# Optimization experiments

Hardware: AMD Instinct MI355X
Metric: run time of the kernel (lower is better)

## Reference

```python
import jax, jax.numpy as jnp
import numpy as np

N_NODES = 100000
N_EDGES = 1600000
D_IN = 128
D_HID = 128
D_OUT = 10
N_GRAPHS = 512


def setup_inputs() -> dict:
    key = jax.random.key(0)
    ks = jax.random.split(key, 12)
    x = jax.random.normal(ks[0], (N_NODES, D_IN), dtype=jnp.float32)
    edge_index = jax.random.randint(ks[1], (2, N_EDGES), 0, N_NODES, dtype=jnp.int64)
    batch = jnp.sort(jax.random.randint(ks[2], (N_NODES,), 0, N_GRAPHS, dtype=jnp.int64))
    s = 1.0 / np.sqrt(D_HID)
    W0 = jax.random.normal(ks[3], (D_HID, D_IN), dtype=jnp.float32) * s
    b0 = jax.random.normal(ks[4], (D_HID,), dtype=jnp.float32) * s
    W1 = jax.random.normal(ks[5], (D_HID, D_HID), dtype=jnp.float32) * s
    b1 = jax.random.normal(ks[6], (D_HID,), dtype=jnp.float32) * s
    W2 = jax.random.normal(ks[7], (D_HID, D_HID), dtype=jnp.float32) * s
    b2 = jax.random.normal(ks[8], (D_HID,), dtype=jnp.float32) * s
    Wg = jax.random.normal(ks[9], (D_OUT, D_HID), dtype=jnp.float32) * s
    bg = jax.random.normal(ks[10], (D_OUT,), dtype=jnp.float32) * s
    return {"x": x, "edge_index": edge_index, "batch": batch,
            "W0": W0, "b0": b0, "W1": W1, "b1": b1, "W2": W2, "b2": b2,
            "Wg": Wg, "bg": bg}


def _gin_conv(x, src, dst, W, b):
    # GINConv with eps=0: Linear(x + sum_{j in N(i)} x_j)
    agg = jax.ops.segment_sum(x[src], dst, num_segments=N_NODES)  # [N, d]
    return (x + agg) @ W.T + b


def reference(x, edge_index, batch, W0, b0, W1, b1, W2, b2, Wg, bg):
    src, dst = edge_index[0], edge_index[1]
    h = jax.nn.relu(_gin_conv(x, src, dst, W0, b0))
    h = jax.nn.relu(_gin_conv(h, src, dst, W1, b1))
    h = _gin_conv(h, src, dst, W2, b2)
    # global_mean_pool over graph ids
    sums = jax.ops.segment_sum(h, batch, num_segments=N_GRAPHS)            # [G, d]
    counts = jax.ops.segment_sum(jnp.ones((N_NODES,), h.dtype), batch, num_segments=N_GRAPHS)
    pooled = sums / jnp.maximum(counts, 1.0)[:, None]                       # [G, d]
    return pooled @ Wg.T + bg                                               # [G, out]
```

## Files before the change

### kernel.cpp

```cpp
#include <hip/hip_runtime.h>

#define N_NODES 100000
#define N_EDGES 1600000
#define N_GRAPHS 512
#define NBUCK 391
#define EPB 8192
#define NB_SCAT ((N_EDGES + EPB - 1) / EPB)
#define CAPB 4864
#define CAP 5120
#define CONV_BLKS 6250
#define AGG_BLKS 2048

typedef _Float16 half8 __attribute__((ext_vector_type(8)));
typedef float floatx4 __attribute__((ext_vector_type(4)));

union U16 { uint4 u; half8 h; };

__global__ __launch_bounds__(256) void convert_pack(const float4* __restrict__ X4,
                                                    uint4* __restrict__ Xh,
                                                    const float* __restrict__ W0,
                                                    const float* __restrict__ W1,
                                                    const float* __restrict__ W2,
                                                    uint4* __restrict__ Bp) {
    int bid = blockIdx.x, tid = threadIdx.x;
    if (bid < CONV_BLKS) {
        int t = bid * 256 + tid;
        float4 a = X4[t * 2], b = X4[t * 2 + 1];
        U16 o;
        o.h[0] = (_Float16)a.x; o.h[1] = (_Float16)a.y;
        o.h[2] = (_Float16)a.z; o.h[3] = (_Float16)a.w;
        o.h[4] = (_Float16)b.x; o.h[5] = (_Float16)b.y;
        o.h[6] = (_Float16)b.z; o.h[7] = (_Float16)b.w;
        Xh[t] = o.u;
    } else {
        int slice = (bid - CONV_BLKS) * 4 + (tid >> 6);
        if (slice >= 96) return;
        int l = tid & 63;
        int layer = slice >> 5;
        int r = slice & 31;
        int c = r >> 3, f = r & 7;
        const float* W = (layer == 0) ? W0 : (layer == 1) ? W1 : W2;
        int col = f * 16 + (l & 15);
        int k0 = c * 32 + (l >> 4) * 8;
        U16 o;
        #pragma unroll
        for (int j = 0; j < 8; ++j) o.h[j] = (_Float16)W[col * 128 + k0 + j];
        Bp[layer * 2048 + (c * 8 + f) * 64 + l] = o.u;
    }
}

__global__ __launch_bounds__(256) void bucket_scatter(const int* __restrict__ src,
                                                      const int* __restrict__ dst,
                                                      int* __restrict__ gcur,
                                                      unsigned* __restrict__ pairs) {
    __shared__ int cnt[NBUCK];
    __shared__ int base[NBUCK];
    int tid = threadIdx.x;
    for (int i = tid; i < NBUCK; i += 256) cnt[i] = 0;
    __syncthreads();
    int e0 = blockIdx.x * EPB, e1 = min(e0 + EPB, N_EDGES);
    for (int e = e0 + tid; e < e1; e += 256) atomicAdd(&cnt[dst[e] >> 8], 1);
    __syncthreads();
    for (int i = tid; i < NBUCK; i += 256) {
        int v = cnt[i];
        base[i] = i * CAPB + (v ? atomicAdd(&gcur[i], v) : 0);
        cnt[i] = 0;
    }
    __syncthreads();
    for (int e = e0 + tid; e < e1; e += 256) {
        int d = dst[e], b = d >> 8;
        int r = atomicAdd(&cnt[b], 1);
        pairs[base[b] + r] = (unsigned)src[e] | ((unsigned)(d & 255) << 17);
    }
}

__global__ __launch_bounds__(256) void bucket_fine(const unsigned* __restrict__ pairs,
                                                   const int* __restrict__ gcur,
                                                   int* __restrict__ off,
                                                   int* __restrict__ srclist) {
    __shared__ int snap[NBUCK];
    __shared__ int ncnt[256];
    __shared__ int ws[4];
    __shared__ int stage[CAP];
    int tid = threadIdx.x, b = blockIdx.x;
    int lane = tid & 63, w = tid >> 6;

    for (int i = tid; i < NBUCK; i += 256) snap[i] = gcur[i];
    ncnt[tid] = 0;
    __syncthreads();
    if (tid < 64) {
        int carry = 0;
        for (int base = 0; base < NBUCK; base += 64) {
            int i = base + tid;
            int v = (i < NBUCK) ? snap[i] : 0;
            int incl = v;
            #pragma unroll
            for (int s = 1; s < 64; s <<= 1) {
                int y = __shfl_up(incl, s, 64);
                if (tid >= s) incl += y;
            }
            if (i < NBUCK) snap[i] = carry + incl - v;
            carry += __shfl(incl, 63, 64);
        }
    }
    __syncthreads();
    int eLo = snap[b];
    int eNext = (b == NBUCK - 1) ? N_EDGES : snap[b + 1];
    int m = eNext - eLo;
    int sb = b * CAPB;
    if (b == 0 && tid == 0) off[N_NODES] = N_EDGES;
    __syncthreads();

    for (int t = tid; t < m; t += 256) {
        unsigned p = pairs[sb + t];
        atomicAdd(&ncnt[(p >> 17) & 255], 1);
    }
    __syncthreads();
    int v = ncnt[tid];
    int incl = v;
    #pragma unroll
    for (int s = 1; s < 64; s <<= 1) { int y = __shfl_up(incl, s, 64); if (lane >= s) incl += y; }
    if (lane == 63) ws[w] = incl;
    __syncthreads();
    if (tid < 4) {
        int t = ws[tid];
        #pragma unroll
        for (int s = 1; s < 4; s <<= 1) { int y = __shfl_up(t, s, 64); if (tid >= s) t += y; }
        ws[tid] = t;
    }
    __syncthreads();
    int excl = (w ? ws[w - 1] : 0) + incl - v;
    int n = (b << 8) + tid;
    if (n < N_NODES) off[n] = eLo + excl;
    __syncthreads();
    ncnt[tid] = excl;
    __syncthreads();
    for (int t = tid; t < m; t += 256) {
        unsigned p = pairs[sb + t];
        int r = atomicAdd(&ncnt[(p >> 17) & 255], 1);
        int s = (int)(p & 0x1FFFFu);
        if (r < CAP) stage[r] = s;
        else srclist[eLo + r] = s;
    }
    __syncthreads();
    int lim = m < CAP ? m : CAP;
    for (int t = tid; t < lim; t += 256) srclist[eLo + t] = stage[t];
}

__global__ __launch_bounds__(256) void agg_f16(const uint4* __restrict__ Xh,
                                               uint4* __restrict__ Ah,
                                               const int* __restrict__ off,
                                               const int* __restrict__ srclist) {
    int t0 = blockIdx.x * 256 + threadIdx.x;
    int c = t0 & 15;
    const int stride = (AGG_BLKS * 256) >> 4;
    for (int n = t0 >> 4; n < N_NODES; n += stride) {
        int j0 = off[n], j1 = off[n + 1];
        U16 acc; acc.u = Xh[(size_t)n * 16 + c];
        half8 a = acc.h;
        for (int j = j0; j < j1; j += 8) {
            int idx[8]; unsigned msk[8];
            #pragma unroll
            for (int i = 0; i < 8; ++i) {
                int jj = j + i;
                bool ok = jj < j1;
                int s = srclist[jj];
                idx[i] = ok ? s : n;
                msk[i] = ok ? 0xFFFFFFFFu : 0u;
            }
            U16 v[8];
            #pragma unroll
            for (int i = 0; i < 8; ++i) v[i].u = Xh[(size_t)idx[i] * 16 + c];
            #pragma unroll
            for (int i = 0; i < 8; ++i) {
                v[i].u.x &= msk[i]; v[i].u.y &= msk[i];
                v[i].u.z &= msk[i]; v[i].u.w &= msk[i];
                a += v[i].h;
            }
        }
        U16 o; o.h = a;
        Ah[(size_t)n * 16 + c] = o.u;
    }
}

__global__ __launch_bounds__(256) void gemm_mfma(const _Float16* __restrict__ Ah,
                                                 const uint4* __restrict__ Bp,
                                                 const float* __restrict__ bias,
                                                 _Float16* __restrict__ H, int doRelu) {
    int tid = threadIdx.x;
    int wid = tid >> 6, lane = tid & 63;
    int nbase = blockIdx.x * 128 + wid * 32;
    int lrow = lane & 15;
    int lk = (lane >> 4) * 8;
    int row0 = min(nbase + lrow, N_NODES - 1);
    int row1 = min(nbase + 16 + lrow, N_NODES - 1);

    floatx4 acc[2][8];
    #pragma unroll
    for (int r = 0; r < 2; ++r)
        #pragma unroll
        for (int f = 0; f < 8; ++f) acc[r][f] = (floatx4)0.f;

    #pragma unroll
    for (int c = 0; c < 4; ++c) {
        U16 a0, a1;
        a0.u = *(const uint4*)(Ah + (size_t)row0 * 128 + c * 32 + lk);
        a1.u = *(const uint4*)(Ah + (size_t)row1 * 128 + c * 32 + lk);
        #pragma unroll
        for (int f = 0; f < 8; ++f) {
            U16 b; b.u = Bp[(c * 8 + f) * 64 + lane];
            acc[0][f] = __builtin_amdgcn_mfma_f32_16x16x32_f16(a0.h, b.h, acc[0][f], 0, 0, 0);
            acc[1][f] = __builtin_amdgcn_mfma_f32_16x16x32_f16(a1.h, b.h, acc[1][f], 0, 0, 0);
        }
    }

    int colb = lane & 15;
    int rq = (lane >> 4) * 4;
    #pragma unroll
    for (int f = 0; f < 8; ++f) {
        float bv = bias[f * 16 + colb];
        #pragma unroll
        for (int r = 0; r < 2; ++r) {
            #pragma unroll
            for (int q = 0; q < 4; ++q) {
                int row = nbase + r * 16 + rq + q;
                if (row < N_NODES) {
                    float v = acc[r][f][q] + bv;
                    if (doRelu) v = fmaxf(v, 0.f);
                    H[(size_t)row * 128 + f * 16 + colb] = (_Float16)v;
                }
            }
        }
    }
}

__device__ __forceinline__ int lower_bound_i(const int* a, int n, int val) {
    int lo = 0, hi = n;
    while (lo < hi) {
        int mid = (lo + hi) >> 1;
        if (a[mid] < val) lo = mid + 1; else hi = mid;
    }
    return lo;
}

__global__ __launch_bounds__(256) void pool_kernel(const uint4* __restrict__ Hh,
                                                   const int* __restrict__ batch,
                                                   const float* __restrict__ Wg,
                                                   const float* __restrict__ bg,
                                                   float* __restrict__ out) {
    __shared__ float p[16 * 128];
    __shared__ float pooled[128];
    int g = blockIdx.x, tid = threadIdx.x;
    int c = tid & 15, r = tid >> 4;
    int lo = lower_bound_i(batch, N_NODES, g);
    int hi = lower_bound_i(batch, N_NODES, g + 1);
    float acc[8] = {0, 0, 0, 0, 0, 0, 0, 0};
    for (int i = lo + r; i < hi; i += 16) {
        U16 v; v.u = Hh[(size_t)i * 16 + c];
        #pragma unroll
        for (int k = 0; k < 8; ++k) acc[k] += (float)v.h[k];
    }
    #pragma unroll
    for (int k = 0; k < 8; ++k) p[r * 128 + c * 8 + k] = acc[k];
    __syncthreads();
    if (tid < 128) {
        float s = 0.f;
        #pragma unroll
        for (int q = 0; q < 16; ++q) s += p[q * 128 + tid];
        pooled[tid] = s / fmaxf((float)(hi - lo), 1.0f);
    }
    __syncthreads();
    if (tid < 10) {
        float s = bg[tid];
        #pragma unroll 4
        for (int k = 0; k < 128; ++k) s += pooled[k] * Wg[tid * 128 + k];
        out[g * 10 + tid] = s;
    }
}

extern "C" void kernel_launch(void* const* d_in, const int* in_sizes, int n_in,
                              void* d_out, int out_size, void* d_ws, size_t ws_size,
                              hipStream_t stream) {
    const float* x   = (const float*)d_in[0];
    const int*   ei  = (const int*)d_in[1];
    const int*   bat = (const int*)d_in[2];
    const float* W0  = (const float*)d_in[3];
    const float* b0  = (const float*)d_in[4];
    const float* W1  = (const float*)d_in[5];
    const float* b1  = (const float*)d_in[6];
    const float* W2  = (const float*)d_in[7];
    const float* b2  = (const float*)d_in[8];
    const float* Wg  = (const float*)d_in[9];
    const float* bg  = (const float*)d_in[10];
    float* out = (float*)d_out;

    const int* src = ei;
    const int* dst = ei + N_EDGES;

    char* w = (char*)d_ws;
    _Float16* Ah    = (_Float16*)(w);
    unsigned* pairs = (unsigned*)(w);
    _Float16* P0    = (_Float16*)(w + 25600000);
    _Float16* P1    = (_Float16*)(w + 51200000);
    _Float16* P2    = (_Float16*)(w + 76800000);
    int*    srclist = (int*)(w + 102400000);
    int*    off     = (int*)(w + 108800000);
    uint4*  Bp      = (uint4*)(w + 109300000);
    int*    gcur    = (int*)(w + 109450000);

    hipMemsetAsync(gcur, 0, NBUCK * sizeof(int), stream);

    bucket_scatter<<<NB_SCAT, 256, 0, stream>>>(src, dst, gcur, pairs);
    bucket_fine<<<NBUCK, 256, 0, stream>>>(pairs, gcur, off, srclist);
    convert_pack<<<CONV_BLKS + 24, 256, 0, stream>>>((const float4*)x, (uint4*)P0,
                                                     W0, W1, W2, Bp);

    int gemmGrid = (N_NODES + 127) / 128;

    agg_f16<<<AGG_BLKS, 256, 0, stream>>>((const uint4*)P0, (uint4*)Ah, off, srclist);
    gemm_mfma<<<gemmGrid, 256, 0, stream>>>(Ah, Bp, b0, P1, 1);
    agg_f16<<<AGG_BLKS, 256, 0, stream>>>((const uint4*)P1, (uint4*)Ah, off, srclist);
    gemm_mfma<<<gemmGrid, 256, 0, stream>>>(Ah, Bp + 2048, b1, P2, 1);
    agg_f16<<<AGG_BLKS, 256, 0, stream>>>((const uint4*)P2, (uint4*)Ah, off, srclist);
    gemm_mfma<<<gemmGrid, 256, 0, stream>>>(Ah, Bp + 4096, b2, P0, 0);

    pool_kernel<<<N_GRAPHS, 256, 0, stream>>>((const uint4*)P0, bat, Wg, bg, out);
}
```

Baseline: 341.9 us.

## Simplify aggregation to one node per launch slot and drop LDS staging

The aggregation kernel now maps each group of 16 threads to exactly one node and launches enough blocks to cover all nodes. It replaces the grid-stride loop and 8-wide masked gather with a 4-way unrolled loop plus a tail. Bucket fine-sort writes source indices directly to global memory instead of staging them in shared memory, and the coarse scatter uses smaller edge chunks per block. This removes masking overhead and LDS usage, but exposes fewer outstanding gathers per thread and uncoalesced scatter writes.

```diff
diff --git a/kernel.cpp b/kernel.cpp
--- a/kernel.cpp
+++ b/kernel.cpp
@@ -4,12 +4,10 @@
 #define N_EDGES 1600000
 #define N_GRAPHS 512
 #define NBUCK 391
-#define EPB 8192
+#define EPB 2048
 #define NB_SCAT ((N_EDGES + EPB - 1) / EPB)
 #define CAPB 4864
-#define CAP 5120
 #define CONV_BLKS 6250
-#define AGG_BLKS 2048
 
 typedef _Float16 half8 __attribute__((ext_vector_type(8)));
 typedef float floatx4 __attribute__((ext_vector_type(4)));
@@ -81,7 +79,6 @@
     __shared__ int snap[NBUCK];
     __shared__ int ncnt[256];
     __shared__ int ws[4];
-    __shared__ int stage[CAP];
     int tid = threadIdx.x, b = blockIdx.x;
     int lane = tid & 63, w = tid >> 6;
 
@@ -138,49 +135,36 @@
     for (int t = tid; t < m; t += 256) {
         unsigned p = pairs[sb + t];
         int r = atomicAdd(&ncnt[(p >> 17) & 255], 1);
-        int s = (int)(p & 0x1FFFFu);
-        if (r < CAP) stage[r] = s;
-        else srclist[eLo + r] = s;
-    }
-    __syncthreads();
-    int lim = m < CAP ? m : CAP;
-    for (int t = tid; t < lim; t += 256) srclist[eLo + t] = stage[t];
+        srclist[eLo + r] = (int)(p & 0x1FFFFu);
+    }
 }
 
 __global__ __launch_bounds__(256) void agg_f16(const uint4* __restrict__ Xh,
                                                uint4* __restrict__ Ah,
                                                const int* __restrict__ off,
                                                const int* __restrict__ srclist) {
-    int t0 = blockIdx.x * 256 + threadIdx.x;
-    int c = t0 & 15;
-    const int stride = (AGG_BLKS * 256) >> 4;
-    for (int n = t0 >> 4; n < N_NODES; n += stride) {
-        int j0 = off[n], j1 = off[n + 1];
-        U16 acc; acc.u = Xh[(size_t)n * 16 + c];
-        half8 a = acc.h;
-        for (int j = j0; j < j1; j += 8) {
-            int idx[8]; unsigned msk[8];
-            #pragma unroll
-            for (int i = 0; i < 8; ++i) {
-                int jj = j + i;
-                bool ok = jj < j1;
-                int s = srclist[jj];
-                idx[i] = ok ? s : n;
-                msk[i] = ok ? 0xFFFFFFFFu : 0u;
-            }
-            U16 v[8];
-            #pragma unroll
-            for (int i = 0; i < 8; ++i) v[i].u = Xh[(size_t)idx[i] * 16 + c];
-            #pragma unroll
-            for (int i = 0; i < 8; ++i) {
-                v[i].u.x &= msk[i]; v[i].u.y &= msk[i];
-                v[i].u.z &= msk[i]; v[i].u.w &= msk[i];
-                a += v[i].h;
-            }
-        }
-        U16 o; o.h = a;
-        Ah[(size_t)n * 16 + c] = o.u;
-    }
+    int t = blockIdx.x * 256 + threadIdx.x;
+    int n = t >> 4, c = t & 15;
+    if (n >= N_NODES) return;
+    int j0 = off[n], j1 = off[n + 1];
+    U16 acc; acc.u = Xh[(size_t)n * 16 + c];
+    half8 a = acc.h;
+    int j = j0;
+    for (; j + 3 < j1; j += 4) {
+        int s0 = srclist[j], s1 = srclist[j + 1], s2 = srclist[j + 2], s3 = srclist[j + 3];
+        U16 v0, v1, v2, v3;
+        v0.u = Xh[(size_t)s0 * 16 + c];
+        v1.u = Xh[(size_t)s1 * 16 + c];
+        v2.u = Xh[(size_t)s2 * 16 + c];
+        v3.u = Xh[(size_t)s3 * 16 + c];
+        a += v0.h; a += v1.h; a += v2.h; a += v3.h;
+    }
+    for (; j < j1; ++j) {
+        U16 v; v.u = Xh[(size_t)srclist[j] * 16 + c];
+        a += v.h;
+    }
+    U16 o; o.h = a;
+    Ah[(size_t)n * 16 + c] = o.u;
 }
 
 __global__ __launch_bounds__(256) void gemm_mfma(const _Float16* __restrict__ Ah,
@@ -315,13 +299,14 @@
     convert_pack<<<CONV_BLKS + 24, 256, 0, stream>>>((const float4*)x, (uint4*)P0,
                                                      W0, W1, W2, Bp);
 
+    int aggGrid  = (N_NODES * 16 + 255) / 256;
     int gemmGrid = (N_NODES + 127) / 128;
 
-    agg_f16<<<AGG_BLKS, 256, 0, stream>>>((const uint4*)P0, (uint4*)Ah, off, srclist);
+    agg_f16<<<aggGrid, 256, 0, stream>>>((const uint4*)P0, (uint4*)Ah, off, srclist);
     gemm_mfma<<<gemmGrid, 256, 0, stream>>>(Ah, Bp, b0, P1, 1);
-    agg_f16<<<AGG_BLKS, 256, 0, stream>>>((const uint4*)P1, (uint4*)Ah, off, srclist);
+    agg_f16<<<aggGrid, 256, 0, stream>>>((const uint4*)P1, (uint4*)Ah, off, srclist);
     gemm_mfma<<<gemmGrid, 256, 0, stream>>>(Ah, Bp + 2048, b1, P2, 1);
-    agg_f16<<<AGG_BLKS, 256, 0, stream>>>((const uint4*)P2, (uint4*)Ah, off, srclist);
+    agg_f16<<<aggGrid, 256, 0, stream>>>((const uint4*)P2, (uint4*)Ah, off, srclist);
     gemm_mfma<<<gemmGrid, 256, 0, stream>>>(Ah, Bp + 4096, b2, P0, 0);
 
     pool_kernel<<<N_GRAPHS, 256, 0, stream>>>((const uint4*)P0, bat, Wg, bg, out);
```

After: 342.0 us. Within noise of the previous version (+0.0%).
